# Performance work log

Measured on AMD Instinct MI355X. Metric: run time of the kernel, lower is better.

## Reference

```python
import jax, jax.numpy as jnp
import numpy as np

P = 16          # patch size
D = 256         # emb dim
NH = 4          # attention heads
DH = D // NH    # head dim
GS = 4          # LE-fusion group size
EPS = 1e-5
ALPHA = 1.0
DELTA = 1.0
BETA = 1.0


def setup_inputs() -> dict:
    key = jax.random.key(0)
    ks = jax.random.split(key, 12)
    B, C, H, W = 8, 1, 256, 256
    s = 0.02
    return {
        "x": jax.random.normal(ks[0], (B, C, H, W), jnp.float32),
        # patch embed as matmul over flattened patches (equivalent to Conv2d k=s=P)
        "Wp": jax.random.normal(ks[1], (C * P * P, D), jnp.float32) * s,
        "bp": jnp.zeros((D,), jnp.float32),
        "ln_g": jnp.ones((D,), jnp.float32),
        "ln_b": jnp.zeros((D,), jnp.float32),
        "Wq": jax.random.normal(ks[2], (D, D), jnp.float32) * s,
        "bq": jnp.zeros((D,), jnp.float32),
        "Wk": jax.random.normal(ks[3], (D, D), jnp.float32) * s,
        "bk": jnp.zeros((D,), jnp.float32),
        "Wv": jax.random.normal(ks[4], (D, D), jnp.float32) * s,
        "bv": jnp.zeros((D,), jnp.float32),
        "Wo": jax.random.normal(ks[5], (D, D), jnp.float32) * s,
        "bo": jnp.zeros((D,), jnp.float32),
    }


def _forward(x, Wp, bp, ln_g, ln_b, Wq, bq, Wk, bk, Wv, bv, Wo, bo):
    B, C, H, W = x.shape
    nh, nw = H // P, W // P
    N = nh * nw
    # --- patch embed: (B,C,H,W) -> (B,N,C*P*P) @ Wp ---
    patches = x.reshape(B, C, nh, P, nw, P).transpose(0, 2, 4, 1, 3, 5)
    patches = patches.reshape(B, N, C * P * P)
    z = patches @ Wp + bp  # (B, N, D)
    # --- NF-Norm: LayerNorm then NeuroFocal scaling ---
    mu = z.mean(-1, keepdims=True)
    var = ((z - mu) ** 2).mean(-1, keepdims=True)
    zn = (z - mu) * jax.lax.rsqrt(var + EPS) * ln_g + ln_b
    mu2 = zn.mean(-1, keepdims=True)
    var2 = ((zn - mu2) ** 2).mean(-1, keepdims=True)
    nf = jnp.abs(zn - mu2).sum(-1, keepdims=True) / (jnp.sqrt(var2 + EPS) + EPS)
    z = zn * (1.0 + nf)
    # --- AG-NFA attention ---
    def split(t):  # (B,N,D) -> (B,NH,N,DH)
        return t.reshape(B, N, NH, DH).transpose(0, 2, 1, 3)
    Q = split(z @ Wq + bq)
    K = split(z @ Wk + bk)
    V = split(z @ Wv + bv)
    qk = jnp.einsum("bhnd,bhmd->bhnm", Q, K)
    logits = qk / jnp.sqrt(jnp.float32(DH))
    mu_q = Q.mean(-1, keepdims=True)
    var_q = ((Q - mu_q) ** 2).mean(-1, keepdims=True)
    sigma_q = jnp.sqrt(var_q + EPS)
    nf_q = jnp.abs(Q - mu_q).sum(-1, keepdims=True) / (sigma_q + EPS)  # (B,NH,N,1)
    # ||Q_n - K_m||^2 = |Q|^2 + |K|^2 - 2 Q.K  (avoids O(N^2*d) diff tensor)
    q2 = (Q * Q).sum(-1)  # (B,NH,N)
    k2 = (K * K).sum(-1)  # (B,NH,N)
    omega = q2[..., :, None] + k2[..., None, :] - 2.0 * qk
    omega = omega / (jnp.exp(-DELTA * nf_q) + 1.0)
    A = jax.nn.softmax(logits - ALPHA * omega, axis=-1)
    out = jnp.einsum("bhnm,bhmd->bhnd", A, V)
    out = out.transpose(0, 2, 1, 3).reshape(B, N, D)
    Y = out @ Wo + bo
    # --- LE-Fusion ---
    G = N // GS
    Yg = Y.reshape(B, G, GS, D)
    E = jnp.linalg.norm(Yg, axis=-1)  # (B,G,GS)
    lam = jax.nn.softmax(BETA * E, axis=-1)[..., None]
    return (lam * Yg).sum(axis=2)  # (B, G, D)


def reference(x, Wp, bp, ln_g, ln_b, Wq, bq, Wk, bk, Wv, bv, Wo, bo):
    return _forward(x, Wp, bp, ln_g, ln_b, Wq, bq, Wk, bk, Wv, bv, Wo, bo)
```

## Files before the change

kernel.cpp:

```cpp
#include <hip/hip_runtime.h>

#define EPSF 1e-5f
#define KSTR 68
#define PSTR 260

#define FMA4(ACC, ZS, WV) \
    ACC.x = fmaf(ZS, WV.x, ACC.x); ACC.y = fmaf(ZS, WV.y, ACC.y); \
    ACC.z = fmaf(ZS, WV.z, ACC.z); ACC.w = fmaf(ZS, WV.w, ACC.w);

__device__ __forceinline__ void pass8x8(
    const float* __restrict__ W, const float* __restrict__ zr,
    float* __restrict__ ps, int kq, int ln)
{
    const float* wr = W + kq * 8192 + 4 * ln;
    const float* zb = zr + kq * 32;
    float4 a0 = make_float4(0.f,0.f,0.f,0.f), a1 = a0, a2 = a0, a3 = a0;
    float4 a4 = a0, a5 = a0, a6 = a0, a7 = a0;
    #pragma unroll
    for (int kk = 0; kk < 32; kk += 4) {
        float4 w0 = *(const float4*)(wr + (kk + 0) * 256);
        float4 w1 = *(const float4*)(wr + (kk + 1) * 256);
        float4 w2 = *(const float4*)(wr + (kk + 2) * 256);
        float4 w3 = *(const float4*)(wr + (kk + 3) * 256);
        float4 z0 = *(const float4*)(zb + 0 * 256 + kk);
        float4 z1 = *(const float4*)(zb + 1 * 256 + kk);
        float4 z2 = *(const float4*)(zb + 2 * 256 + kk);
        float4 z3 = *(const float4*)(zb + 3 * 256 + kk);
        float4 z4 = *(const float4*)(zb + 4 * 256 + kk);
        float4 z5 = *(const float4*)(zb + 5 * 256 + kk);
        float4 z6 = *(const float4*)(zb + 6 * 256 + kk);
        float4 z7 = *(const float4*)(zb + 7 * 256 + kk);
        FMA4(a0, z0.x, w0) FMA4(a0, z0.y, w1) FMA4(a0, z0.z, w2) FMA4(a0, z0.w, w3)
        FMA4(a1, z1.x, w0) FMA4(a1, z1.y, w1) FMA4(a1, z1.z, w2) FMA4(a1, z1.w, w3)
        FMA4(a2, z2.x, w0) FMA4(a2, z2.y, w1) FMA4(a2, z2.z, w2) FMA4(a2, z2.w, w3)
        FMA4(a3, z3.x, w0) FMA4(a3, z3.y, w1) FMA4(a3, z3.z, w2) FMA4(a3, z3.w, w3)
        FMA4(a4, z4.x, w0) FMA4(a4, z4.y, w1) FMA4(a4, z4.z, w2) FMA4(a4, z4.w, w3)
        FMA4(a5, z5.x, w0) FMA4(a5, z5.y, w1) FMA4(a5, z5.z, w2) FMA4(a5, z5.w, w3)
        FMA4(a6, z6.x, w0) FMA4(a6, z6.y, w1) FMA4(a6, z6.z, w2) FMA4(a6, z6.w, w3)
        FMA4(a7, z7.x, w0) FMA4(a7, z7.y, w1) FMA4(a7, z7.z, w2) FMA4(a7, z7.w, w3)
    }
    float* pp = ps + kq * 2048 + 4 * ln;
    *(float4*)(pp + 0 * 256) = a0;
    *(float4*)(pp + 1 * 256) = a1;
    *(float4*)(pp + 2 * 256) = a2;
    *(float4*)(pp + 3 * 256) = a3;
    *(float4*)(pp + 4 * 256) = a4;
    *(float4*)(pp + 5 * 256) = a5;
    *(float4*)(pp + 6 * 256) = a6;
    *(float4*)(pp + 7 * 256) = a7;
}

__device__ __forceinline__ float4 combine8(const float* __restrict__ ps, int e)
{
    float4 a = *(const float4*)(ps + e);
    #pragma unroll
    for (int k = 1; k < 8; ++k) {
        float4 u = *(const float4*)(ps + k * 2048 + e);
        a.x += u.x; a.y += u.y; a.z += u.z; a.w += u.w;
    }
    return a;
}

__global__ __launch_bounds__(512, 2) void ka_patch_nf_qkv(
    const float* __restrict__ x,
    const float* __restrict__ Wp, const float* __restrict__ bp,
    const float* __restrict__ ln_g, const float* __restrict__ ln_b,
    const float* __restrict__ Wq, const float* __restrict__ bq,
    const float* __restrict__ Wk, const float* __restrict__ bk,
    const float* __restrict__ Wv, const float* __restrict__ bv,
    float* __restrict__ Qg, float* __restrict__ Kg, float* __restrict__ Vg)
{
    extern __shared__ float sm[];
    float* zr  = sm;
    float* psA = sm + 2048;
    float* psB = sm + 18432;

    const int tid = threadIdx.x;
    const int kq = tid >> 6, ln = tid & 63;
    const int lane = tid & 63;
    const int tok0 = blockIdx.x * 8;

    {
        int e = tid * 4;
        int t = e >> 8, dd = e & 255;
        int tk = tok0 + t, b = tk >> 8, n = tk & 255;
        int ph = n >> 4, pw = n & 15, p = (dd >> 4) & 15, q = dd & 15;
        *(float4*)(zr + e) =
            *(const float4*)(x + b * 65536 + (ph * 16 + p) * 256 + pw * 16 + q);
    }
    __syncthreads();

    pass8x8(Wp, zr, psA, kq, ln);
    __syncthreads();

    {
        int e = tid * 4;
        float4 a = combine8(psA, e);
        float4 bb = *(const float4*)(bp + 4 * lane);
        a.x += bb.x; a.y += bb.y; a.z += bb.z; a.w += bb.w;

        float s  = a.x + a.y + a.z + a.w;
        float ss = a.x*a.x + a.y*a.y + a.z*a.z + a.w*a.w;
        #pragma unroll
        for (int o = 32; o; o >>= 1) { s += __shfl_xor(s, o); ss += __shfl_xor(ss, o); }
        float mu  = s * (1.f / 256.f);
        float var = ss * (1.f / 256.f) - mu * mu;
        float rs  = rsqrtf(var + EPSF);

        float4 g  = *(const float4*)(ln_g + 4 * lane);
        float4 b2 = *(const float4*)(ln_b + 4 * lane);
        float4 zn;
        zn.x = (a.x - mu) * rs * g.x + b2.x;
        zn.y = (a.y - mu) * rs * g.y + b2.y;
        zn.z = (a.z - mu) * rs * g.z + b2.z;
        zn.w = (a.w - mu) * rs * g.w + b2.w;

        float s2  = zn.x + zn.y + zn.z + zn.w;
        float ss2 = zn.x*zn.x + zn.y*zn.y + zn.z*zn.z + zn.w*zn.w;
        #pragma unroll
        for (int o = 32; o; o >>= 1) { s2 += __shfl_xor(s2, o); ss2 += __shfl_xor(ss2, o); }
        float mu2  = s2 * (1.f / 256.f);
        float var2 = ss2 * (1.f / 256.f) - mu2 * mu2;

        float as = fabsf(zn.x - mu2) + fabsf(zn.y - mu2)
                 + fabsf(zn.z - mu2) + fabsf(zn.w - mu2);
        #pragma unroll
        for (int o = 32; o; o >>= 1) as += __shfl_xor(as, o);
        float nf = as / (sqrtf(var2 + EPSF) + EPSF);
        float sc = 1.f + nf;
        zn.x *= sc; zn.y *= sc; zn.z *= sc; zn.w *= sc;
        *(float4*)(zr + e) = zn;
    }
    __syncthreads();

    int e = tid * 4, t = e >> 8, d0 = e & 255;
    int tk = tok0 + t, b = tk >> 8, n = tk & 255;
    int h = d0 >> 6, dh = d0 & 63;
    const long goff = ((long)(b * 4 + h) * 256 + n) * 64 + dh;

    pass8x8(Wq, zr, psB, kq, ln);
    __syncthreads();

    {
        float4 a = combine8(psB, e);
        float4 bb = *(const float4*)(bq + d0);
        a.x += bb.x; a.y += bb.y; a.z += bb.z; a.w += bb.w;
        *(float4*)(Qg + goff) = a;
    }
    pass8x8(Wk, zr, psA, kq, ln);
    __syncthreads();

    {
        float4 a = combine8(psA, e);
        float4 bb = *(const float4*)(bk + d0);
        a.x += bb.x; a.y += bb.y; a.z += bb.z; a.w += bb.w;
        *(float4*)(Kg + goff) = a;
    }
    pass8x8(Wv, zr, psB, kq, ln);
    __syncthreads();

    {
        float4 a = combine8(psB, e);
        float4 bb = *(const float4*)(bv + d0);
        a.x += bb.x; a.y += bb.y; a.z += bb.z; a.w += bb.w;
        *(float4*)(Vg + goff) = a;
    }
}

__global__ __launch_bounds__(512, 2) void kb_attn(
    const float* __restrict__ Qg, const float* __restrict__ Kg,
    const float* __restrict__ Vg, float* __restrict__ Og)
{
    extern __shared__ float lds[];
    float* Kl = lds;
    float* Vl = lds + 256 * KSTR;
    float* k2 = lds + 2 * 256 * KSTR;
    float* Pl = Kl;

    const int tid = threadIdx.x;
    const int xcd = blockIdx.x & 7, slot = blockIdx.x >> 3;
    const int bh = xcd * 4 + (slot >> 3);
    const int qt = slot & 7;

    const float* Qb = Qg + (bh * 256 + qt * 32) * 64;
    const float* Kb = Kg + bh * 16384;
    const float* Vb = Vg + bh * 16384;

    const int q = tid >> 4;
    const int r = tid & 15;

    {
        const float4* Ks = (const float4*)Kb;
        const float4* Vs = (const float4*)Vb;
        #pragma unroll
        for (int i = 0; i < 8; ++i) {
            int flat = tid + 512 * i;
            int row = flat >> 4, c4 = flat & 15;
            *(float4*)(Kl + row * KSTR + c4 * 4) = Ks[flat];
            *(float4*)(Vl + row * KSTR + c4 * 4) = Vs[flat];
        }
    }
    __syncthreads();

    {
        int row = tid >> 1, half = tid & 1;
        const float* kp = Kl + row * KSTR + half * 32;
        float ssq = 0.f;
        #pragma unroll
        for (int c = 0; c < 8; ++c) {
            float4 kv = *(const float4*)(kp + 4 * c);
            ssq += kv.x*kv.x + kv.y*kv.y + kv.z*kv.z + kv.w*kv.w;
        }
        ssq += __shfl_xor(ssq, 1);
        if (half == 0) k2[row] = ssq;
    }

    float4 Qr[16];
    {
        const float4* Qp = (const float4*)(Qb + q * 64);
        #pragma unroll
        for (int c = 0; c < 16; ++c) Qr[c] = Qp[c];
    }
    float fq, gq, iq;
    {
        float s = 0.f, ss = 0.f;
        #pragma unroll
        for (int c = 0; c < 16; ++c) {
            float4 v = Qr[c];
            s  += v.x + v.y + v.z + v.w;
            ss += v.x*v.x + v.y*v.y + v.z*v.z + v.w*v.w;
        }
        float mu = s * (1.f / 64.f);
        float as = 0.f;
        #pragma unroll
        for (int c = 0; c < 16; ++c) {
            float4 v = Qr[c];
            as += fabsf(v.x - mu) + fabsf(v.y - mu)
                + fabsf(v.z - mu) + fabsf(v.w - mu);
        }
        float var = ss * (1.f / 64.f) - mu * mu;
        float sg  = sqrtf(var + EPSF);
        float nf  = as / (sg + EPSF);
        float inv = 1.f / (__expf(-nf) + 1.f);
        fq = 0.125f + 2.f * inv;
        gq = ss * inv;
        iq = inv;
    }
    __syncthreads();

    float s_[16];
    #pragma unroll
    for (int j = 0; j < 16; ++j) {
        int m = r + 16 * j;
        const float* kp = Kl + m * KSTR;
        float acc = 0.f;
        #pragma unroll
        for (int c = 0; c < 16; ++c) {
            float4 kv = *(const float4*)(kp + 4 * c);
            acc += Qr[c].x*kv.x + Qr[c].y*kv.y + Qr[c].z*kv.z + Qr[c].w*kv.w;
        }
        s_[j] = acc * fq - gq - k2[m] * iq;
    }

    float M = s_[0];
    #pragma unroll
    for (int j = 1; j < 16; ++j) M = fmaxf(M, s_[j]);
    #pragma unroll
    for (int o = 1; o < 16; o <<= 1) M = fmaxf(M, __shfl_xor(M, o));
    float L = 0.f;
    #pragma unroll
    for (int j = 0; j < 16; ++j) { s_[j] = __expf(s_[j] - M); L += s_[j]; }
    #pragma unroll
    for (int o = 1; o < 16; o <<= 1) L += __shfl_xor(L, o);
    float invL = 1.f / L;

    __syncthreads();
    #pragma unroll
    for (int j = 0; j < 16; ++j) Pl[q * PSTR + r + 16 * j] = s_[j] * invL;
    __syncthreads();

    float4 a0 = make_float4(0.f, 0.f, 0.f, 0.f);
    const float* pq = Pl + q * PSTR;
    const float* vp = Vl + 4 * r;
    #pragma unroll 8
    for (int m = 0; m < 256; ++m) {
        float pw = pq[m];
        float4 v = *(const float4*)(vp + m * KSTR);
        a0.x = fmaf(pw, v.x, a0.x); a0.y = fmaf(pw, v.y, a0.y);
        a0.z = fmaf(pw, v.z, a0.z); a0.w = fmaf(pw, v.w, a0.w);
    }
    {
        int b = bh >> 2, h = bh & 3;
        int n = qt * 32 + q;
        float* op = Og + (b * 256 + n) * 256 + h * 64 + 4 * r;
        *(float4*)op = a0;
    }
}

__global__ __launch_bounds__(512, 2) void kc_wo_le(
    const float* __restrict__ Og, const float* __restrict__ Wo,
    const float* __restrict__ bo, float* __restrict__ out)
{
    extern __shared__ float sm[];
    float* yr  = sm;
    float* ps  = sm + 2048;
    float* red = sm + 18432;

    const int tid = threadIdx.x;
    const int kq = tid >> 6, ln = tid & 63;
    const int wave = tid >> 6, lane = tid & 63;
    const int tok0 = blockIdx.x * 8;

    *(float4*)(yr + tid * 4) = *(const float4*)(Og + tok0 * 256 + tid * 4);
    __syncthreads();

    pass8x8(Wo, yr, ps, kq, ln);
    __syncthreads();

    {
        int e = tid * 4;
        float4 a = combine8(ps, e);
        float4 bb = *(const float4*)(bo + 4 * lane);
        a.x += bb.x; a.y += bb.y; a.z += bb.z; a.w += bb.w;
        float ssq = a.x*a.x + a.y*a.y + a.z*a.z + a.w*a.w;
        #pragma unroll
        for (int o = 32; o; o >>= 1) ssq += __shfl_xor(ssq, o);
        if (lane == 0) red[wave] = sqrtf(ssq);
        *(float4*)(yr + e) = a;
    }
    __syncthreads();

    {
        int g = tid >> 8, d = tid & 255;
        float e0 = red[4 * g], e1 = red[4 * g + 1], e2 = red[4 * g + 2], e3 = red[4 * g + 3];
        float m = fmaxf(fmaxf(e0, e1), fmaxf(e2, e3));
        float x0 = __expf(e0 - m), x1 = __expf(e1 - m), x2 = __expf(e2 - m), x3 = __expf(e3 - m);
        float inv = 1.f / (x0 + x1 + x2 + x3);
        float val = (x0 * yr[(4 * g) * 256 + d] + x1 * yr[(4 * g + 1) * 256 + d]
                   + x2 * yr[(4 * g + 2) * 256 + d] + x3 * yr[(4 * g + 3) * 256 + d]) * inv;
        out[(blockIdx.x * 2 + g) * 256 + d] = val;
    }
}

extern "C" void kernel_launch(void* const* d_in, const int* in_sizes, int n_in,
                              void* d_out, int out_size, void* d_ws, size_t ws_size,
                              hipStream_t stream) {
    const float* x    = (const float*)d_in[0];
    const float* Wp   = (const float*)d_in[1];
    const float* bp   = (const float*)d_in[2];
    const float* ln_g = (const float*)d_in[3];
    const float* ln_b = (const float*)d_in[4];
    const float* Wq   = (const float*)d_in[5];
    const float* bq   = (const float*)d_in[6];
    const float* Wk   = (const float*)d_in[7];
    const float* bk   = (const float*)d_in[8];
    const float* Wv   = (const float*)d_in[9];
    const float* bv   = (const float*)d_in[10];
    const float* Wo   = (const float*)d_in[11];
    const float* bo   = (const float*)d_in[12];
    float* out = (float*)d_out;

    float* ws = (float*)d_ws;
    float* Qg = ws;
    float* Kg = ws + 524288;
    float* Vg = ws + 524288 * 2;
    float* Og = ws + 524288 * 3;

    const int ka_lds = (2048 + 2 * 16384) * 4;
    const int kb_lds = (2 * 256 * KSTR + 256) * 4;
    const int kc_lds = (2048 + 16384 + 8) * 4;
    (void)hipFuncSetAttribute((const void*)ka_patch_nf_qkv,
                              hipFuncAttributeMaxDynamicSharedMemorySize, ka_lds);
    (void)hipFuncSetAttribute((const void*)kb_attn,
                              hipFuncAttributeMaxDynamicSharedMemorySize, kb_lds);
    (void)hipFuncSetAttribute((const void*)kc_wo_le,
                              hipFuncAttributeMaxDynamicSharedMemorySize, kc_lds);

    ka_patch_nf_qkv<<<256, 512, ka_lds, stream>>>(x, Wp, bp, ln_g, ln_b,
                                                  Wq, bq, Wk, bk, Wv, bv, Qg, Kg, Vg);
    kb_attn<<<256, 512, kb_lds, stream>>>(Qg, Kg, Vg, Og);
    kc_wo_le<<<256, 512, kc_lds, stream>>>(Og, Wo, bo, out);
}
```

Measured before the change: 49.73 us.

## Split attention head dimension across thread pairs with 1024-thread blocks

Doubles the attention block to 1024 threads and assigns two threads per query/output slot. Each handles half of the head dimension for QK and half of the keys for PV, and the partial results are combined with cross-lane shuffles. This halves the per-thread serial work and the Q register footprint, which should raise parallelism and latency hiding. The cost is extra shuffles, duplicated softmax math across the thread pair, and a launch_bounds of (1024,4) that may force register spilling.

```diff
diff --git a/kernel.cpp b/kernel.cpp
--- a/kernel.cpp
+++ b/kernel.cpp
@@ -167,7 +167,7 @@
     }
 }
 
-__global__ __launch_bounds__(512, 2) void kb_attn(
+__global__ __launch_bounds__(1024, 4) void kb_attn(
     const float* __restrict__ Qg, const float* __restrict__ Kg,
     const float* __restrict__ Vg, float* __restrict__ Og)
 {
@@ -186,15 +186,17 @@
     const float* Kb = Kg + bh * 16384;
     const float* Vb = Vg + bh * 16384;
 
-    const int q = tid >> 4;
-    const int r = tid & 15;
+    const int q   = tid >> 5;
+    const int r   = tid & 31;
+    const int rlo = r & 15;
+    const int rhi = r >> 4;
 
     {
         const float4* Ks = (const float4*)Kb;
         const float4* Vs = (const float4*)Vb;
         #pragma unroll
-        for (int i = 0; i < 8; ++i) {
-            int flat = tid + 512 * i;
+        for (int i = 0; i < 4; ++i) {
+            int flat = tid + 1024 * i;
             int row = flat >> 4, c4 = flat & 15;
             *(float4*)(Kl + row * KSTR + c4 * 4) = Ks[flat];
             *(float4*)(Vl + row * KSTR + c4 * 4) = Vs[flat];
@@ -203,30 +205,28 @@
     __syncthreads();
 
     {
-        int row = tid >> 1, half = tid & 1;
-        const float* kp = Kl + row * KSTR + half * 32;
+        int row = tid >> 2, part = tid & 3;
+        const float* kp = Kl + row * KSTR + part * 16;
         float ssq = 0.f;
         #pragma unroll
-        for (int c = 0; c < 8; ++c) {
+        for (int c = 0; c < 4; ++c) {
             float4 kv = *(const float4*)(kp + 4 * c);
             ssq += kv.x*kv.x + kv.y*kv.y + kv.z*kv.z + kv.w*kv.w;
         }
         ssq += __shfl_xor(ssq, 1);
-        if (half == 0) k2[row] = ssq;
-    }
-
-    float4 Qr[16];
+        ssq += __shfl_xor(ssq, 2);
+        if (part == 0) k2[row] = ssq;
+    }
+
+    float fq, gq, iq;
     {
         const float4* Qp = (const float4*)(Qb + q * 64);
-        #pragma unroll
-        for (int c = 0; c < 16; ++c) Qr[c] = Qp[c];
-    }
-    float fq, gq, iq;
-    {
         float s = 0.f, ss = 0.f;
+        float4 vbuf[16];
         #pragma unroll
         for (int c = 0; c < 16; ++c) {
-            float4 v = Qr[c];
+            float4 v = Qp[c];
+            vbuf[c] = v;
             s  += v.x + v.y + v.z + v.w;
             ss += v.x*v.x + v.y*v.y + v.z*v.z + v.w*v.w;
         }
@@ -234,7 +234,7 @@
         float as = 0.f;
         #pragma unroll
         for (int c = 0; c < 16; ++c) {
-            float4 v = Qr[c];
+            float4 v = vbuf[c];
             as += fabsf(v.x - mu) + fabsf(v.y - mu)
                 + fabsf(v.z - mu) + fabsf(v.w - mu);
         }
@@ -246,19 +246,27 @@
         gq = ss * inv;
         iq = inv;
     }
+
+    float4 Qh[8];
+    {
+        const float4* Qp = (const float4*)(Qb + q * 64) + rhi * 8;
+        #pragma unroll
+        for (int c = 0; c < 8; ++c) Qh[c] = Qp[c];
+    }
     __syncthreads();
 
     float s_[16];
     #pragma unroll
     for (int j = 0; j < 16; ++j) {
-        int m = r + 16 * j;
-        const float* kp = Kl + m * KSTR;
+        int m = rlo + 16 * j;
+        const float* kp = Kl + m * KSTR + rhi * 32;
         float acc = 0.f;
         #pragma unroll
-        for (int c = 0; c < 16; ++c) {
+        for (int c = 0; c < 8; ++c) {
             float4 kv = *(const float4*)(kp + 4 * c);
-            acc += Qr[c].x*kv.x + Qr[c].y*kv.y + Qr[c].z*kv.z + Qr[c].w*kv.w;
-        }
+            acc += Qh[c].x*kv.x + Qh[c].y*kv.y + Qh[c].z*kv.z + Qh[c].w*kv.w;
+        }
+        acc += __shfl_xor(acc, 16);
         s_[j] = acc * fq - gq - k2[m] * iq;
     }
 
@@ -275,24 +283,30 @@
     float invL = 1.f / L;
 
     __syncthreads();
-    #pragma unroll
-    for (int j = 0; j < 16; ++j) Pl[q * PSTR + r + 16 * j] = s_[j] * invL;
+    if (rhi == 0) {
+        #pragma unroll
+        for (int j = 0; j < 16; ++j) Pl[q * PSTR + rlo + 16 * j] = s_[j] * invL;
+    }
     __syncthreads();
 
     float4 a0 = make_float4(0.f, 0.f, 0.f, 0.f);
-    const float* pq = Pl + q * PSTR;
-    const float* vp = Vl + 4 * r;
+    const float* pq = Pl + q * PSTR + rhi * 128;
+    const float* vp = Vl + rhi * 128 * KSTR + 4 * rlo;
     #pragma unroll 8
-    for (int m = 0; m < 256; ++m) {
+    for (int m = 0; m < 128; ++m) {
         float pw = pq[m];
         float4 v = *(const float4*)(vp + m * KSTR);
         a0.x = fmaf(pw, v.x, a0.x); a0.y = fmaf(pw, v.y, a0.y);
         a0.z = fmaf(pw, v.z, a0.z); a0.w = fmaf(pw, v.w, a0.w);
     }
-    {
+    a0.x += __shfl_xor(a0.x, 16);
+    a0.y += __shfl_xor(a0.y, 16);
+    a0.z += __shfl_xor(a0.z, 16);
+    a0.w += __shfl_xor(a0.w, 16);
+    if (rhi == 0) {
         int b = bh >> 2, h = bh & 3;
         int n = qt * 32 + q;
-        float* op = Og + (b * 256 + n) * 256 + h * 64 + 4 * r;
+        float* op = Og + (b * 256 + n) * 256 + h * 64 + 4 * rlo;
         *(float4*)op = a0;
     }
 }
@@ -378,6 +392,6 @@
 
     ka_patch_nf_qkv<<<256, 512, ka_lds, stream>>>(x, Wp, bp, ln_g, ln_b,
                                                   Wq, bq, Wk, bk, Wv, bv, Qg, Kg, Vg);
-    kb_attn<<<256, 512, kb_lds, stream>>>(Qg, Kg, Vg, Og);
+    kb_attn<<<256, 1024, kb_lds, stream>>>(Qg, Kg, Vg, Og);
     kc_wo_le<<<256, 512, kc_lds, stream>>>(Og, Wo, bo, out);
 }
```

Result: slower. 55.11 us (+10.8%).
